# Optimization experiments

Measured on AMD Instinct MI355X. Metric: run time of the kernel, lower is better.

Reference implementation:

```python
import jax, jax.numpy as jnp
import numpy as np

H = 768      # hidden_size
NH = 12      # num_attention_heads
DH = H // NH # attention_head_size
FF = 3072    # intermediate_size
E = 4        # n_expert
B, S = 8, 512
EPS = 1e-12


def _layernorm(x, g, b):
    mu = jnp.mean(x, axis=-1, keepdims=True)
    var = jnp.var(x, axis=-1, keepdims=True)
    return (x - mu) * jax.lax.rsqrt(var + EPS) * g + b


def _expert_linear(x, W, b, expert_idx):
    # W: [E, in, out], b: [E, out]; gather per-sample expert weights, then batched GEMM.
    # Mathematically identical to running every expert then slicing (single_select_fwd).
    Wg = W[expert_idx]            # [B, in, out]
    bg = b[expert_idx]            # [B, out]
    return jnp.einsum('bsi,bio->bso', x, Wg) + bg[:, None, :]


def setup_inputs() -> dict:
    key = jax.random.key(0)
    ks = jax.random.split(key, 16)
    sc = 0.02
    inp = {
        'hidden_states': jax.random.normal(ks[0], (B, S, H), jnp.float32),
        'expert_idx': jax.random.randint(ks[1], (B,), 0, E, jnp.int64) if jax.config.read('jax_enable_x64') else jax.random.randint(ks[1], (B,), 0, E).astype(jnp.int32),
        'attention_mask': jnp.zeros((B, 1, 1, S), jnp.float32),
        'Wq': sc * jax.random.normal(ks[2], (E, H, H), jnp.float32),
        'bq': jnp.zeros((E, H), jnp.float32),
        'Wk': sc * jax.random.normal(ks[3], (E, H, H), jnp.float32),
        'bk': jnp.zeros((E, H), jnp.float32),
        'Wv': sc * jax.random.normal(ks[4], (E, H, H), jnp.float32),
        'bv': jnp.zeros((E, H), jnp.float32),
        'Wo': sc * jax.random.normal(ks[5], (E, H, H), jnp.float32),
        'bo': jnp.zeros((E, H), jnp.float32),
        'ln1_g': jnp.ones((H,), jnp.float32),
        'ln1_b': jnp.zeros((H,), jnp.float32),
        'Wi': sc * jax.random.normal(ks[6], (E, H, FF), jnp.float32),
        'bi': jnp.zeros((E, FF), jnp.float32),
        'Wout': sc * jax.random.normal(ks[7], (E, FF, H), jnp.float32),
        'bout': jnp.zeros((E, H), jnp.float32),
        'ln2_g': jnp.ones((H,), jnp.float32),
        'ln2_b': jnp.zeros((H,), jnp.float32),
    }
    return inp


def reference(hidden_states, expert_idx, attention_mask, Wq, bq, Wk, bk, Wv, bv,
              Wo, bo, ln1_g, ln1_b, Wi, bi, Wout, bout, ln2_g, ln2_b):
    b, s, h = hidden_states.shape
    # --- MoE self-attention (per-sample expert QKV) ---
    q = _expert_linear(hidden_states, Wq, bq, expert_idx).reshape(b, s, NH, DH).transpose(0, 2, 1, 3)
    k = _expert_linear(hidden_states, Wk, bk, expert_idx).reshape(b, s, NH, DH).transpose(0, 2, 1, 3)
    v = _expert_linear(hidden_states, Wv, bv, expert_idx).reshape(b, s, NH, DH).transpose(0, 2, 1, 3)
    scores = jnp.einsum('bhqd,bhkd->bhqk', q, k) / np.sqrt(DH).astype(np.float32)
    scores = scores + attention_mask
    probs = jax.nn.softmax(scores, axis=-1)
    ctx = jnp.einsum('bhqk,bhkd->bhqd', probs, v).transpose(0, 2, 1, 3).reshape(b, s, h)
    # --- MoE self-output: dense + residual + LN ---
    attn_out = _expert_linear(ctx, Wo, bo, expert_idx)
    x = _layernorm(attn_out + hidden_states, ln1_g, ln1_b)
    # --- MoE FFN: intermediate (GELU) + output + residual + LN ---
    hmid = jax.nn.gelu(_expert_linear(x, Wi, bi, expert_idx), approximate=False)
    ffn = _expert_linear(hmid, Wout, bout, expert_idx)
    return _layernorm(ffn + x, ln2_g, ln2_b)
```

## Files before the change

kernel.cpp:

```cpp
#include <hip/hip_runtime.h>
#include <cstdint>
#include <cstddef>

constexpr int CB  = 8;
constexpr int CS  = 512;
constexpr int CH  = 768;
constexpr int CNH = 12;
constexpr int CDH = 64;
constexpr int CFF = 3072;
constexpr int CE  = 4;
constexpr int C3H = 3 * CH;

using f32x4  = __attribute__((ext_vector_type(4))) float;
using bf16x8 = __attribute__((ext_vector_type(8))) short;

__device__ __forceinline__ short f2bf(float x) {
  union { float f; uint32_t u; } v; v.f = x;
  return (short)((v.u + 0x7fffu + ((v.u >> 16) & 1u)) >> 16);
}

__device__ __forceinline__ void gload_lds16(const void* g, void* l) {
  __builtin_amdgcn_global_load_lds((const __attribute__((address_space(1))) void*)g,
                                   (__attribute__((address_space(3))) void*)l,
                                   16, 0, 0);
}

#define VMCNT(n)  asm volatile("s_waitcnt vmcnt(" #n ")" ::: "memory")
#define SCHEDB()  __builtin_amdgcn_sched_barrier(0)

__global__ void cvt_bf16_kernel(const float* __restrict__ in, short* __restrict__ out, int n4) {
  int i = blockIdx.x * blockDim.x + threadIdx.x;
  if (i < n4) {
    float4 v = ((const float4*)in)[i];
    short4 o;
    o.x = f2bf(v.x); o.y = f2bf(v.y); o.z = f2bf(v.z); o.w = f2bf(v.w);
    ((short4*)out)[i] = o;
  }
}

__device__ __forceinline__ bool expert_used(const int* __restrict__ eidx, int e) {
  bool u = false;
#pragma unroll
  for (int s = 0; s < CB; ++s) u |= (eidx[s] == e);
  return u;
}

__device__ __forceinline__ void tpose_body(const float* __restrict__ Wb,
                                           short* __restrict__ Wtb, int K, int N) {
  __shared__ __align__(16) short Ts[64 * 68];
  const int n0 = blockIdx.x * 64, k0 = blockIdx.y * 64;
  const int t  = threadIdx.x;
  const int tn = t & 15, tk = t >> 4;
#pragma unroll
  for (int p = 0; p < 4; ++p) {
    int k = k0 + p * 16 + tk;
    float4 v = *(const float4*)(Wb + (size_t)k * N + n0 + tn * 4);
#pragma unroll
    for (int j = 0; j < 4; ++j)
      Ts[(tn * 4 + j) * 68 + p * 16 + tk] = f2bf(((const float*)&v)[j]);
  }
  __syncthreads();
#pragma unroll
  for (int p = 0; p < 4; ++p) {
    int n = n0 + p * 16 + tk;
    uint2 o = *(const uint2*)(Ts + (p * 16 + tk) * 68 + tn * 4);
    *(uint2*)(Wtb + (size_t)n * K + k0 + tn * 4) = o;
  }
}

__global__ void tpose_cvt_kernel(const float* __restrict__ W, short* __restrict__ Wt,
                                 const int* __restrict__ eidx, int K, int N) {
  const int e = blockIdx.z;
  if (!expert_used(eidx, e)) return;
  tpose_body(W + (size_t)e * K * N, Wt + (size_t)e * K * N, K, N);
}

__global__ void tpose4_kernel(const float* __restrict__ Wq, const float* __restrict__ Wk,
                              const float* __restrict__ Wv, const float* __restrict__ Wo,
                              const int* __restrict__ eidx,
                              short* __restrict__ Wqkvt, short* __restrict__ Wot) {
  const int z = blockIdx.z, e = z >> 2, m = z & 3;
  if (!expert_used(eidx, e)) return;
  const float* W = (m == 0) ? Wq : (m == 1) ? Wk : (m == 2) ? Wv : Wo;
  const float* Wb = W + (size_t)e * CH * CH;
  short* dst = (m == 3) ? (Wot + (size_t)e * CH * CH)
                        : (Wqkvt + ((size_t)e * C3H + m * CH) * CH);
  tpose_body(Wb, dst, CH, CH);
}

__global__ void qkv_bias_kernel(const float* __restrict__ bq, const float* __restrict__ bk,
                                const float* __restrict__ bv, float* __restrict__ dst) {
  int i = blockIdx.x * 256 + threadIdx.x;
  if (i >= CE * C3H) return;
  int e = i / C3H, r = i % C3H;
  int m = r / CH, c = r % CH;
  const float* s = (m == 0) ? bq : (m == 1) ? bk : bv;
  dst[i] = s[e * CH + c];
}

template <int BM, int NTN, int KSPLIT, int NJB, int NNB>
__device__ __forceinline__ void moe_decode(const int* __restrict__ eidx,
                                           int& e, int& mrow0, int& nt, int& ks) {
  constexpr int JC  = 4096 / BM;
  constexpr int MTS = CS / BM;
  constexpr int CHJ = JC / NJB;
  constexpr int CHN = NTN / NNB;
  constexpr int NKB = 8 / (NJB * NNB);
  constexpr int CHK = KSPLIT / NKB;
  int exv[CB];
#pragma unroll
  for (int s = 0; s < CB; ++s) exv[s] = eidx[s];
  uint32_t epack = 0;
#pragma unroll
  for (int s = 0; s < CB; ++s) epack |= (uint32_t)exv[s] << (2 * s);
  int c0 = 0, c1 = 0, c2 = 0;
#pragma unroll
  for (int s = 0; s < CB; ++s) {
    c0 += (exv[s] == 0); c1 += (exv[s] == 1); c2 += (exv[s] == 2);
  }
  int p0 = 0, p1 = c0, p2 = c0 + c1, p3 = c0 + c1 + c2;
  uint32_t sortedPack = 0;
#pragma unroll
  for (int s = 0; s < CB; ++s) {
    int ee = exv[s];
    int p = (ee == 0) ? p0 : (ee == 1) ? p1 : (ee == 2) ? p2 : p3;
    sortedPack |= (uint32_t)s << (4 * p);
    p0 += (ee == 0); p1 += (ee == 1); p2 += (ee == 2); p3 += (ee == 3);
  }
  const int x = (int)blockIdx.x & 7;
  const int i = (int)blockIdx.x >> 3;
  const int kb = x / (NJB * NNB);
  const int rx = x - kb * (NJB * NNB);
  const int jb = rx / NNB, nb = rx - (rx / NNB) * NNB;
  const int nn = i % CHN;
  const int rem = i / CHN;
  const int jj = rem % CHJ;
  const int kk2 = rem / CHJ;
  const int j = jb * CHJ + jj;
  nt = nb * CHN + nn;
  ks = kb * CHK + kk2;
  const int sample = (int)((sortedPack >> (4 * (j / MTS))) & 7);
  e = (int)((epack >> (2 * sample)) & 3);
  mrow0 = sample * CS + (j % MTS) * BM;
}

template <int K, int NTN, int KSPLIT, int NJB, int NNB, int ACT, bool OB16>
__global__ __launch_bounds__(256, 2)
void gemm8_kernel(const short* __restrict__ A, const short* __restrict__ Wt,
                  const float* __restrict__ bias, const int* __restrict__ eidx,
                  char* __restrict__ out, char* __restrict__ out2,
                  size_t wtExpStride, int biasStride, int outLd, size_t outKsStride) {
  constexpr int BM = 128, BN = 192;
  constexpr int MI = 4, NI = 6;
  constexpr int NT = K / KSPLIT / 128;
  __shared__ __align__(16) short As[BM * 128];
  __shared__ __align__(16) short Bs[BN * 128];
  const int t = threadIdx.x, w = t >> 6, l = t & 63, lr = l & 15, lg = l >> 4;

  int e, mrow0, nt, ks;
  moe_decode<BM, NTN, KSPLIT, NJB, NNB>(eidx, e, mrow0, nt, ks);
  const int kBase = ks * NT * 128;

  const int srow = t >> 4;
  const int gcol = ((t & 15) ^ srow) * 8;
  const short* aSrc = A + (size_t)(mrow0 + srow) * K + kBase + gcol;
  const short* bSrc = Wt + (size_t)e * wtExpStride + (size_t)(nt * BN + srow) * K + kBase + gcol;
  const size_t iss16 = (size_t)16 * K;

  const int wrow = (w >> 1) * 64, wn = (w & 1) * 96;
  int aoff[4][MI], boff[4][NI];
#pragma unroll
  for (int kk = 0; kk < 4; ++kk) {
    const int c = (kk * 4 + lg) ^ lr;
#pragma unroll
    for (int mi = 0; mi < MI; ++mi)
      aoff[kk][mi] = (wrow + mi * 16 + lr) * 128 + c * 8;
#pragma unroll
    for (int ni = 0; ni < NI; ++ni)
      boff[kk][ni] = (wn + ni * 16 + lr) * 128 + c * 8;
  }

  f32x4 acc[MI][NI] = {};

  for (int kt = 0; kt < NT; ++kt) {
    {
      const short* as = aSrc + (size_t)kt * 128;
#pragma unroll
      for (int i = 0; i < 8; ++i)
        gload_lds16(as + i * iss16, &As[i * 2048 + t * 8]);
      const short* bs = bSrc + (size_t)kt * 128;
#pragma unroll
      for (int i = 0; i < 12; ++i)
        gload_lds16(bs + i * iss16, &Bs[i * 2048 + t * 8]);
    }
    VMCNT(0);
    __builtin_amdgcn_s_barrier();
    SCHEDB();
#pragma unroll
    for (int kk = 0; kk < 4; ++kk) {
      bf16x8 af[MI], bfr[NI];
#pragma unroll
      for (int ni = 0; ni < NI; ++ni) bfr[ni] = *(const bf16x8*)(&Bs[boff[kk][ni]]);
#pragma unroll
      for (int mi = 0; mi < MI; ++mi) af[mi] = *(const bf16x8*)(&As[aoff[kk][mi]]);
      __builtin_amdgcn_s_setprio(1);
#pragma unroll
      for (int mi = 0; mi < MI; ++mi)
#pragma unroll
        for (int ni = 0; ni < NI; ++ni)
          acc[mi][ni] = __builtin_amdgcn_mfma_f32_16x16x32_bf16(af[mi], bfr[ni],
                                                                acc[mi][ni], 0, 0, 0);
      __builtin_amdgcn_s_setprio(0);
    }
    __builtin_amdgcn_s_barrier();
    SCHEDB();
  }

  float* outF = (ks < 2) ? ((float*)out + (size_t)ks * outKsStride)
                         : ((float*)out2 + (size_t)(ks - 2) * outKsStride);
#pragma unroll
  for (int ni = 0; ni < NI; ++ni) {
    const int col = nt * BN + wn + ni * 16 + lr;
    const float bv = bias ? bias[e * biasStride + col] : 0.0f;
#pragma unroll
    for (int mi = 0; mi < MI; ++mi) {
      const int row0 = mrow0 + wrow + mi * 16 + lg * 4;
#pragma unroll
      for (int r = 0; r < 4; ++r) {
        float v = acc[mi][ni][r] + bv;
        if (ACT == 1) v = 0.5f * v * (1.0f + erff(v * 0.70710678118654752f));
        if (OB16) ((short*)out)[(size_t)(row0 + r) * outLd + col] = f2bf(v);
        else      outF[(size_t)(row0 + r) * outLd + col] = v;
      }
    }
  }
}

__global__ void attn_kernel(const short* __restrict__ QKV, const float* __restrict__ mask,
                            short* __restrict__ ctx) {
  __shared__ __align__(16) short Vt[2][64 * 40];
  __shared__ __align__(16) short Pt[4][2][16 * 40];
  const int bh = blockIdx.x;
  const int b = bh / CNH, h = bh % CNH;
  const int qt = blockIdx.y;
  const int t = threadIdx.x, w = t >> 6, l = t & 63, lr = l & 15, lg = l >> 4;

  const size_t bS = (size_t)b * CS;
  const short* Qh = QKV + bS * C3H + h * CDH;
  const short* Kh = Qh + CH;
  const short* Vh = Qh + 2 * CH;
  const float* mrow = mask + bS;

  const int qrow = qt * 64 + w * 16 + lr;
  bf16x8 qa[2];
  qa[0] = *(const bf16x8*)(Qh + (size_t)qrow * C3H + lg * 8);
  qa[1] = *(const bf16x8*)(Qh + (size_t)qrow * C3H + 32 + lg * 8);

  f32x4 o[4] = {};
  float lp[4] = {0.f, 0.f, 0.f, 0.f};

  const int dh = t & 63, kg = t >> 6;
  {
    short v8[8];
#pragma unroll
    for (int j = 0; j < 8; ++j) v8[j] = Vh[(size_t)(kg * 8 + j) * C3H + dh];
    uint32_t p0 = (uint32_t)(uint16_t)v8[0] | ((uint32_t)(uint16_t)v8[1] << 16);
    uint32_t p1 = (uint32_t)(uint16_t)v8[2] | ((uint32_t)(uint16_t)v8[3] << 16);
    uint32_t p2 = (uint32_t)(uint16_t)v8[4] | ((uint32_t)(uint16_t)v8[5] << 16);
    uint32_t p3 = (uint32_t)(uint16_t)v8[6] | ((uint32_t)(uint16_t)v8[7] << 16);
    uint4 pk = {p0, p1, p2, p3};
    *(uint4*)(&Vt[0][dh * 40 + kg * 8]) = pk;
  }

  for (int tt = 0; tt < CS / 32; ++tt) {
    const int k0 = tt * 32;
    __syncthreads();

    f32x4 sacc[2] = {};
#pragma unroll
    for (int n = 0; n < 2; ++n) {
      bf16x8 kb0 = *(const bf16x8*)(Kh + (size_t)(k0 + n * 16 + lr) * C3H + lg * 8);
      bf16x8 kb1 = *(const bf16x8*)(Kh + (size_t)(k0 + n * 16 + lr) * C3H + 32 + lg * 8);
      sacc[n] = __builtin_amdgcn_mfma_f32_16x16x32_bf16(qa[0], kb0, sacc[n], 0, 0, 0);
      sacc[n] = __builtin_amdgcn_mfma_f32_16x16x32_bf16(qa[1], kb1, sacc[n], 0, 0, 0);
    }

    if (tt + 1 < CS / 32) {
      const int k1 = k0 + 32;
      short v8[8];
#pragma unroll
      for (int j = 0; j < 8; ++j) v8[j] = Vh[(size_t)(k1 + kg * 8 + j) * C3H + dh];
      uint32_t p0 = (uint32_t)(uint16_t)v8[0] | ((uint32_t)(uint16_t)v8[1] << 16);
      uint32_t p1 = (uint32_t)(uint16_t)v8[2] | ((uint32_t)(uint16_t)v8[3] << 16);
      uint32_t p2 = (uint32_t)(uint16_t)v8[4] | ((uint32_t)(uint16_t)v8[5] << 16);
      uint32_t p3 = (uint32_t)(uint16_t)v8[6] | ((uint32_t)(uint16_t)v8[7] << 16);
      uint4 pk = {p0, p1, p2, p3};
      *(uint4*)(&Vt[(tt + 1) & 1][dh * 40 + kg * 8]) = pk;
    }

    const int pb = tt & 1;
#pragma unroll
    for (int n = 0; n < 2; ++n) {
      float mv = mrow[k0 + n * 16 + lr];
#pragma unroll
      for (int r = 0; r < 4; ++r) {
        float s = sacc[n][r] * 0.125f + mv;
        float e = __expf(s);
        lp[r] += e;
        Pt[w][pb][(lg * 4 + r) * 40 + n * 16 + lr] = f2bf(e);
      }
    }

    bf16x8 pa = *(const bf16x8*)(&Pt[w][pb][lr * 40 + lg * 8]);
#pragma unroll
    for (int d = 0; d < 4; ++d) {
      bf16x8 vbf = *(const bf16x8*)(&Vt[tt & 1][(d * 16 + lr) * 40 + lg * 8]);
      o[d] = __builtin_amdgcn_mfma_f32_16x16x32_bf16(pa, vbf, o[d], 0, 0, 0);
    }
  }

#pragma unroll
  for (int r = 0; r < 4; ++r) {
    float s = lp[r];
    s += __shfl_xor(s, 1); s += __shfl_xor(s, 2);
    s += __shfl_xor(s, 4); s += __shfl_xor(s, 8);
    lp[r] = 1.0f / s;
  }
#pragma unroll
  for (int d = 0; d < 4; ++d)
#pragma unroll
    for (int r = 0; r < 4; ++r) {
      int row = qt * 64 + w * 16 + lg * 4 + r;
      ctx[(bS + row) * CH + h * CDH + d * 16 + lr] = f2bf(o[d][r] * lp[r]);
    }
}

template <int NP>
__global__ void ln12_kernel(const float* __restrict__ p0, const float* __restrict__ p1,
                            const float* __restrict__ p2, const float* __restrict__ p3,
                            const float* __restrict__ res,
                            const float* __restrict__ btab, const int* __restrict__ eidx,
                            const float* __restrict__ g, const float* __restrict__ bta,
                            float* __restrict__ out32, short* __restrict__ out16) {
  const int row = blockIdx.x;
  const int l = threadIdx.x;
  const int e = eidx[row >> 9];
  const float* xr0 = p0 + (size_t)row * CH;
  const float* xr1 = p1 + (size_t)row * CH;
  const float* rr  = res + (size_t)row * CH;
  const float* bo  = btab + (size_t)e * CH;
  float4 v[3];
  float sum = 0.f, ss = 0.f;
#pragma unroll
  for (int j = 0; j < 3; ++j) {
    float4 a = *(const float4*)(xr0 + j * 256 + l * 4);
    float4 c = *(const float4*)(xr1 + j * 256 + l * 4);
    float4 b = *(const float4*)(rr + j * 256 + l * 4);
    float4 bb = *(const float4*)(bo + j * 256 + l * 4);
    a.x += c.x + b.x + bb.x; a.y += c.y + b.y + bb.y;
    a.z += c.z + b.z + bb.z; a.w += c.w + b.w + bb.w;
    if (NP == 4) {
      float4 d2 = *(const float4*)(p2 + (size_t)row * CH + j * 256 + l * 4);
      float4 d3 = *(const float4*)(p3 + (size_t)row * CH + j * 256 + l * 4);
      a.x += d2.x + d3.x; a.y += d2.y + d3.y;
      a.z += d2.z + d3.z; a.w += d2.w + d3.w;
    }
    v[j] = a;
    sum += a.x + a.y + a.z + a.w;
    ss  += a.x * a.x + a.y * a.y + a.z * a.z + a.w * a.w;
  }
#pragma unroll
  for (int m = 1; m < 64; m <<= 1) { sum += __shfl_xor(sum, m); ss += __shfl_xor(ss, m); }
  const float mean = sum * (1.0f / CH);
  const float var  = ss * (1.0f / CH) - mean * mean;
  const float rstd = rsqrtf(var + 1e-12f);
#pragma unroll
  for (int j = 0; j < 3; ++j) {
    float4 gg = *(const float4*)(g   + j * 256 + l * 4);
    float4 bb = *(const float4*)(bta + j * 256 + l * 4);
    float4 a = v[j], y;
    y.x = (a.x - mean) * rstd * gg.x + bb.x;
    y.y = (a.y - mean) * rstd * gg.y + bb.y;
    y.z = (a.z - mean) * rstd * gg.z + bb.z;
    y.w = (a.w - mean) * rstd * gg.w + bb.w;
    *(float4*)(out32 + (size_t)row * CH + j * 256 + l * 4) = y;
    if (out16) {
      short4 o;
      o.x = f2bf(y.x); o.y = f2bf(y.y); o.z = f2bf(y.z); o.w = f2bf(y.w);
      *(short4*)(out16 + (size_t)row * CH + j * 256 + l * 4) = o;
    }
  }
}

extern "C" void kernel_launch(void* const* d_in, const int* in_sizes, int n_in,
                              void* d_out, int out_size, void* d_ws, size_t ws_size,
                              hipStream_t stream) {
  (void)in_sizes; (void)n_in; (void)out_size; (void)ws_size;
  const float* hidden = (const float*)d_in[0];
  const int*   eidx   = (const int*)d_in[1];
  const float* mask   = (const float*)d_in[2];
  const float* Wq   = (const float*)d_in[3];
  const float* bq   = (const float*)d_in[4];
  const float* Wk   = (const float*)d_in[5];
  const float* bk   = (const float*)d_in[6];
  const float* Wv   = (const float*)d_in[7];
  const float* bv   = (const float*)d_in[8];
  const float* Wo   = (const float*)d_in[9];
  const float* bo   = (const float*)d_in[10];
  const float* ln1g = (const float*)d_in[11];
  const float* ln1b = (const float*)d_in[12];
  const float* Wi   = (const float*)d_in[13];
  const float* bi   = (const float*)d_in[14];
  const float* Wout = (const float*)d_in[15];
  const float* bout = (const float*)d_in[16];
  const float* ln2g = (const float*)d_in[17];
  const float* ln2b = (const float*)d_in[18];

  char* ws = (char*)d_ws;
  size_t off = 0;
  auto alloc = [&](size_t bytes) {
    void* p = ws + off;
    off += (bytes + 255) & ~(size_t)255;
    return p;
  };
  const size_t M = (size_t)CB * CS;
  short* Xb    = (short*)alloc(M * CH * 2);
  char*  Rbig  = (char*)alloc(M * CFF * 2);
  char*  Rcx   = (char*)alloc(M * CH * 4);
  float* parts = (float*)alloc(2 * M * CH * 4);
  float* qkvbias = (float*)alloc(CE * C3H * 4);
  short* Wqkvt = (short*)alloc((size_t)CE * C3H * CH * 2);
  short* Wot   = (short*)alloc((size_t)CE * CH * CH * 2);
  short* Wit   = (short*)alloc((size_t)CE * CH * CFF * 2);
  short* Wo2t  = (short*)alloc((size_t)CE * CFF * CH * 2);
  short* QKVb = (short*)Rbig;
  short* hmid = (short*)Rbig;
  short* ctxb = (short*)Rcx;
  float* x1   = (float*)Rcx;
  short* x1b  = Xb;
  float* pp2  = (float*)Wqkvt;
  float* pp3  = pp2 + M * CH;

  const int n4 = (int)(M * CH / 4);
  cvt_bf16_kernel<<<(n4 + 255) / 256, 256, 0, stream>>>(hidden, Xb, n4);
  tpose4_kernel<<<dim3(CH / 64, CH / 64, 4 * CE), 256, 0, stream>>>(Wq, Wk, Wv, Wo, eidx, Wqkvt, Wot);
  tpose_cvt_kernel<<<dim3(CFF / 64, CH / 64, CE), 256, 0, stream>>>(Wi, Wit, eidx, CH, CFF);
  tpose_cvt_kernel<<<dim3(CH / 64, CFF / 64, CE), 256, 0, stream>>>(Wout, Wo2t, eidx, CFF, CH);
  qkv_bias_kernel<<<(CE * C3H + 255) / 256, 256, 0, stream>>>(bq, bk, bv, qkvbias);

  gemm8_kernel<CH, 12, 1, 4, 2, 0, true><<<384, 256, 0, stream>>>(
      Xb, Wqkvt, qkvbias, eidx, (char*)QKVb, nullptr, (size_t)C3H * CH, C3H, C3H, 0);
  attn_kernel<<<dim3(CB * CNH, CS / 64), 256, 0, stream>>>(QKVb, mask, ctxb);
  gemm8_kernel<CH, 4, 2, 4, 1, 0, false><<<256, 256, 0, stream>>>(
      ctxb, Wot, nullptr, eidx, (char*)parts, nullptr, (size_t)CH * CH, CH, CH, M * CH);
  ln12_kernel<2><<<(int)M, 64, 0, stream>>>(parts, parts + M * CH, nullptr, nullptr,
                                            hidden, bo, eidx, ln1g, ln1b, x1, x1b);
  gemm8_kernel<CH, 16, 1, 4, 2, 1, true><<<512, 256, 0, stream>>>(
      x1b, Wit, bi, eidx, (char*)hmid, nullptr, (size_t)CH * CFF, CFF, CFF, 0);
  gemm8_kernel<CFF, 4, 4, 2, 1, 0, false><<<512, 256, 0, stream>>>(
      hmid, Wo2t, nullptr, eidx, (char*)parts, (char*)pp2, (size_t)CFF * CH, CH, CH, M * CH);
  ln12_kernel<4><<<(int)M, 64, 0, stream>>>(parts, parts + M * CH, pp2, pp3,
                                            x1, bout, eidx, ln2g, ln2b, (float*)d_out, nullptr);
}
```

Measured before the change: 186.5 us.

## Add triple-buffered 256x128 GEMM kernel for QKV and FFN-up projections

```diff
diff --git a/kernel.cpp b/kernel.cpp
--- a/kernel.cpp
+++ b/kernel.cpp
@@ -98,6 +98,30 @@
   dst[i] = s[e * CH + c];
 }
 
+__device__ __forceinline__ void expert_sort(const int* __restrict__ eidx,
+                                            uint32_t& epack, uint32_t& sortedPack) {
+  int exv[CB];
+#pragma unroll
+  for (int s = 0; s < CB; ++s) exv[s] = eidx[s];
+  epack = 0;
+#pragma unroll
+  for (int s = 0; s < CB; ++s) epack |= (uint32_t)exv[s] << (2 * s);
+  int c0 = 0, c1 = 0, c2 = 0;
+#pragma unroll
+  for (int s = 0; s < CB; ++s) {
+    c0 += (exv[s] == 0); c1 += (exv[s] == 1); c2 += (exv[s] == 2);
+  }
+  int p0 = 0, p1 = c0, p2 = c0 + c1, p3 = c0 + c1 + c2;
+  sortedPack = 0;
+#pragma unroll
+  for (int s = 0; s < CB; ++s) {
+    int ee = exv[s];
+    int p = (ee == 0) ? p0 : (ee == 1) ? p1 : (ee == 2) ? p2 : p3;
+    sortedPack |= (uint32_t)s << (4 * p);
+    p0 += (ee == 0); p1 += (ee == 1); p2 += (ee == 2); p3 += (ee == 3);
+  }
+}
+
 template <int BM, int NTN, int KSPLIT, int NJB, int NNB>
 __device__ __forceinline__ void moe_decode(const int* __restrict__ eidx,
                                            int& e, int& mrow0, int& nt, int& ks) {
@@ -107,26 +131,8 @@
   constexpr int CHN = NTN / NNB;
   constexpr int NKB = 8 / (NJB * NNB);
   constexpr int CHK = KSPLIT / NKB;
-  int exv[CB];
-#pragma unroll
-  for (int s = 0; s < CB; ++s) exv[s] = eidx[s];
-  uint32_t epack = 0;
-#pragma unroll
-  for (int s = 0; s < CB; ++s) epack |= (uint32_t)exv[s] << (2 * s);
-  int c0 = 0, c1 = 0, c2 = 0;
-#pragma unroll
-  for (int s = 0; s < CB; ++s) {
-    c0 += (exv[s] == 0); c1 += (exv[s] == 1); c2 += (exv[s] == 2);
-  }
-  int p0 = 0, p1 = c0, p2 = c0 + c1, p3 = c0 + c1 + c2;
-  uint32_t sortedPack = 0;
-#pragma unroll
-  for (int s = 0; s < CB; ++s) {
-    int ee = exv[s];
-    int p = (ee == 0) ? p0 : (ee == 1) ? p1 : (ee == 2) ? p2 : p3;
-    sortedPack |= (uint32_t)s << (4 * p);
-    p0 += (ee == 0); p1 += (ee == 1); p2 += (ee == 2); p3 += (ee == 3);
-  }
+  uint32_t epack, sortedPack;
+  expert_sort(eidx, epack, sortedPack);
   const int x = (int)blockIdx.x & 7;
   const int i = (int)blockIdx.x >> 3;
   const int kb = x / (NJB * NNB);
@@ -142,6 +148,136 @@
   const int sample = (int)((sortedPack >> (4 * (j / MTS))) & 7);
   e = (int)((epack >> (2 * sample)) & 3);
   mrow0 = sample * CS + (j % MTS) * BM;
+}
+
+template <int BM, int NTN>
+__device__ __forceinline__ void moe_decode9(const int* __restrict__ eidx,
+                                            int& e, int& mrow0, int& nt) {
+  constexpr int MTS = CS / BM;
+  uint32_t epack, sortedPack;
+  expert_sort(eidx, epack, sortedPack);
+  const int chunk = (int)gridDim.x >> 3;
+  const int W_ = ((int)blockIdx.x & 7) * chunk + ((int)blockIdx.x >> 3);
+  const int j = W_ / NTN;
+  nt = W_ - j * NTN;
+  const int sample = (int)((sortedPack >> (4 * (j / MTS))) & 7);
+  e = (int)((epack >> (2 * sample)) & 3);
+  mrow0 = sample * CS + (j % MTS) * BM;
+}
+
+template <int K, int NTN, int ACT, bool OB16>
+__global__ __launch_bounds__(512, 1)
+void gemm9_kernel(const short* __restrict__ A, const short* __restrict__ Wt,
+                  const float* __restrict__ bias, const int* __restrict__ eidx,
+                  char* __restrict__ out,
+                  size_t wtExpStride, int biasStride, int outLd) {
+  constexpr int BM = 256, BN = 128;
+  constexpr int NT = K / 64;
+  __shared__ __align__(16) short As[3][BM * 64];
+  __shared__ __align__(16) short Bs[3][BN * 64];
+  const int t = threadIdx.x, w = t >> 6, l = t & 63, lr = l & 15, lg = l >> 4;
+
+  int e, mrow0, nt;
+  moe_decode9<BM, NTN>(eidx, e, mrow0, nt);
+
+  const int srow = t >> 3;
+  const int gcol = (((t & 7) ^ ((t >> 3) & 7)) * 8);
+  const short* aSrc = A + (size_t)(mrow0 + srow) * K + gcol;
+  const short* bSrc = Wt + (size_t)e * wtExpStride + (size_t)(nt * BN + srow) * K + gcol;
+  const size_t iss64 = (size_t)64 * K;
+
+  const int wr = w >> 1, wc = w & 1;
+  int aoff[2][4], boff[2][4];
+#pragma unroll
+  for (int ks = 0; ks < 2; ++ks) {
+    const int slot = (ks * 4 + lg) ^ (lr & 7);
+#pragma unroll
+    for (int mi = 0; mi < 4; ++mi)
+      aoff[ks][mi] = (wr * 64 + mi * 16 + lr) * 64 + slot * 8;
+#pragma unroll
+    for (int ni = 0; ni < 4; ++ni)
+      boff[ks][ni] = (wc * 64 + ni * 16 + lr) * 64 + slot * 8;
+  }
+
+  f32x4 acc[4][4] = {};
+
+  auto STAGE_A9 = [&](int buf, int kt) {
+    const short* as = aSrc + (size_t)kt * 64;
+#pragma unroll
+    for (int i = 0; i < 4; ++i)
+      gload_lds16(as + i * iss64, &As[buf][i * 4096 + t * 8]);
+  };
+  auto STAGE_B9 = [&](int buf, int kt) {
+    const short* bs = bSrc + (size_t)kt * 64;
+#pragma unroll
+    for (int i = 0; i < 2; ++i)
+      gload_lds16(bs + i * iss64, &Bs[buf][i * 4096 + t * 8]);
+  };
+
+  STAGE_A9(0, 0); STAGE_B9(0, 0);
+  STAGE_A9(1, 1); STAGE_B9(1, 1);
+
+  int cb = 0;
+  for (int kt = 0; kt < NT; ++kt) {
+    if (kt == NT - 1) { VMCNT(0); } else { VMCNT(6); }
+    __builtin_amdgcn_s_barrier();
+    SCHEDB();
+    const int sb = (cb == 0) ? 2 : cb - 1;
+    {
+      bf16x8 af[4], bfr[4];
+#pragma unroll
+      for (int ni = 0; ni < 4; ++ni) bfr[ni] = *(const bf16x8*)(&Bs[cb][boff[0][ni]]);
+#pragma unroll
+      for (int mi = 0; mi < 4; ++mi) af[mi] = *(const bf16x8*)(&As[cb][aoff[0][mi]]);
+      if (kt + 2 < NT) STAGE_A9(sb, kt + 2);
+      SCHEDB();
+      __builtin_amdgcn_s_setprio(1);
+#pragma unroll
+      for (int mi = 0; mi < 4; ++mi)
+#pragma unroll
+        for (int ni = 0; ni < 4; ++ni)
+          acc[mi][ni] = __builtin_amdgcn_mfma_f32_16x16x32_bf16(af[mi], bfr[ni],
+                                                                acc[mi][ni], 0, 0, 0);
+      __builtin_amdgcn_s_setprio(0);
+      SCHEDB();
+    }
+    {
+      bf16x8 af[4], bfr[4];
+#pragma unroll
+      for (int ni = 0; ni < 4; ++ni) bfr[ni] = *(const bf16x8*)(&Bs[cb][boff[1][ni]]);
+#pragma unroll
+      for (int mi = 0; mi < 4; ++mi) af[mi] = *(const bf16x8*)(&As[cb][aoff[1][mi]]);
+      if (kt + 2 < NT) STAGE_B9(sb, kt + 2);
+      SCHEDB();
+      __builtin_amdgcn_s_setprio(1);
+#pragma unroll
+      for (int mi = 0; mi < 4; ++mi)
+#pragma unroll
+        for (int ni = 0; ni < 4; ++ni)
+          acc[mi][ni] = __builtin_amdgcn_mfma_f32_16x16x32_bf16(af[mi], bfr[ni],
+                                                                acc[mi][ni], 0, 0, 0);
+      __builtin_amdgcn_s_setprio(0);
+      SCHEDB();
+    }
+    cb = (cb == 2) ? 0 : cb + 1;
+  }
+
+#pragma unroll
+  for (int ni = 0; ni < 4; ++ni) {
+    const int col = nt * BN + wc * 64 + ni * 16 + lr;
+    const float bv = bias ? bias[e * biasStride + col] : 0.0f;
+#pragma unroll
+    for (int mi = 0; mi < 4; ++mi) {
+      const int row0 = mrow0 + wr * 64 + mi * 16 + lg * 4;
+#pragma unroll
+      for (int r = 0; r < 4; ++r) {
+        float v = acc[mi][ni][r] + bv;
+        if (ACT == 1) v = 0.5f * v * (1.0f + erff(v * 0.70710678118654752f));
+        if (OB16) ((short*)out)[(size_t)(row0 + r) * outLd + col] = f2bf(v);
+        else      ((float*)out)[(size_t)(row0 + r) * outLd + col] = v;
+      }
+    }
+  }
 }
 
 template <int K, int NTN, int KSPLIT, int NJB, int NNB, int ACT, bool OB16>
@@ -448,15 +584,15 @@
   tpose_cvt_kernel<<<dim3(CH / 64, CFF / 64, CE), 256, 0, stream>>>(Wout, Wo2t, eidx, CFF, CH);
   qkv_bias_kernel<<<(CE * C3H + 255) / 256, 256, 0, stream>>>(bq, bk, bv, qkvbias);
 
-  gemm8_kernel<CH, 12, 1, 4, 2, 0, true><<<384, 256, 0, stream>>>(
-      Xb, Wqkvt, qkvbias, eidx, (char*)QKVb, nullptr, (size_t)C3H * CH, C3H, C3H, 0);
+  gemm9_kernel<CH, 18, 0, true><<<288, 512, 0, stream>>>(
+      Xb, Wqkvt, qkvbias, eidx, (char*)QKVb, (size_t)C3H * CH, C3H, C3H);
   attn_kernel<<<dim3(CB * CNH, CS / 64), 256, 0, stream>>>(QKVb, mask, ctxb);
   gemm8_kernel<CH, 4, 2, 4, 1, 0, false><<<256, 256, 0, stream>>>(
       ctxb, Wot, nullptr, eidx, (char*)parts, nullptr, (size_t)CH * CH, CH, CH, M * CH);
   ln12_kernel<2><<<(int)M, 64, 0, stream>>>(parts, parts + M * CH, nullptr, nullptr,
                                             hidden, bo, eidx, ln1g, ln1b, x1, x1b);
-  gemm8_kernel<CH, 16, 1, 4, 2, 1, true><<<512, 256, 0, stream>>>(
-      x1b, Wit, bi, eidx, (char*)hmid, nullptr, (size_t)CH * CFF, CFF, CFF, 0);
+  gemm9_kernel<CH, 24, 1, true><<<384, 512, 0, stream>>>(
+      x1b, Wit, bi, eidx, (char*)hmid, (size_t)CH * CFF, CFF, CFF);
   gemm8_kernel<CFF, 4, 4, 2, 1, 0, false><<<512, 256, 0, stream>>>(
       hmid, Wo2t, nullptr, eidx, (char*)parts, (char*)pp2, (size_t)CFF * CH, CH, CH, M * CH);
   ln12_kernel<4><<<(int)M, 64, 0, stream>>>(parts, parts + M * CH, pp2, pp3,
```

Result: slower. 205.5 us (+10.2%).
